# Performance work log

Hardware: AMD Instinct MI355X
Metric: run time of the kernel (lower is better)

Reference implementation:

```python
import jax, jax.numpy as jnp
import numpy as np

B, N, C, H, KHOP = 8, 1024, 512, 16, 2
HD = C // H
VALID = 768          # valid (non-padded) nodes per batch row
E = B * VALID * 32   # ~deg 32 per valid node
BN_EPS = 1e-5
LN_EPS = 1e-5


def setup_inputs() -> dict:
    key = jax.random.key(0)
    ks = jax.random.split(key, 12)
    x = jax.random.normal(ks[0], (B, N, C), jnp.float32)
    shift = jax.random.normal(ks[1], (B, C), jnp.float32) * 0.1
    scale = jax.random.normal(ks[2], (B, C), jnp.float32) * 0.1
    # fixed-size valid prefix per row -> static shapes under jit
    mask = jnp.broadcast_to(jnp.arange(N) < VALID, (B, N))
    # edges live inside a single graph (same batch row), only among valid nodes,
    # expressed directly in flattened [B*N] index space (== compacted indexing up to relabeling)
    eb = jax.random.randint(ks[3], (E,), 0, B)
    es = jax.random.randint(ks[4], (E,), 0, VALID)
    ed = jax.random.randint(ks[5], (E,), 0, VALID)
    edge_index = jnp.stack([eb * N + es, eb * N + ed]).astype(jnp.int32)
    w = lambda k, s: jax.random.normal(k, s, jnp.float32) * 0.02
    gin_eps = jnp.zeros((KHOP,), jnp.float32)
    gin_w1 = w(ks[6], (KHOP, C, 2 * C)); gin_b1 = jnp.zeros((KHOP, 2 * C), jnp.float32)
    gin_bn_g = jnp.ones((KHOP, 2 * C), jnp.float32); gin_bn_b = jnp.zeros((KHOP, 2 * C), jnp.float32)
    gin_w2 = w(ks[7], (KHOP, 2 * C, C)); gin_b2 = jnp.zeros((KHOP, C), jnp.float32)
    ln_g = jnp.ones((C,), jnp.float32); ln_b = jnp.zeros((C,), jnp.float32)
    qkv_w = w(ks[8], (C, 3 * C)); qkv_b = jnp.zeros((3 * C,), jnp.float32)
    proj_w = w(ks[9], (C, C)); proj_b = jnp.zeros((C,), jnp.float32)
    return dict(x=x, shift=shift, scale=scale, mask=mask, edge_index=edge_index,
                gin_eps=gin_eps, gin_w1=gin_w1, gin_b1=gin_b1, gin_bn_g=gin_bn_g,
                gin_bn_b=gin_bn_b, gin_w2=gin_w2, gin_b2=gin_b2, ln_g=ln_g, ln_b=ln_b,
                qkv_w=qkv_w, qkv_b=qkv_b, proj_w=proj_w, proj_b=proj_b)


def _gin_layer(h, mask_f, cnt, src, dst, eps, w1, b1, g, bt, w2, b2):
    # GINConv: mlp((1+eps)*x_i + sum_{j->i} x_j); MLP = Linear->BatchNorm(batch stats over valid nodes)->ReLU->Linear
    agg = jax.ops.segment_sum(h[src], dst, num_segments=B * N)  # scatter-add messages
    z = (1.0 + eps) * h + agg
    pre = z @ w1 + b1                              # [B*N, 2C]
    mw = mask_f[:, None]
    mean = (pre * mw).sum(0) / cnt                 # masked BN statistics (valid nodes only)
    var = (((pre - mean) ** 2) * mw).sum(0) / cnt  # biased var, as torch BatchNorm
    hn = jax.nn.relu(g * (pre - mean) * jax.lax.rsqrt(var + BN_EPS) + bt)
    return (hn @ w2 + b2) * mw                     # zero out padded nodes (x_struct stays 0 there)


def reference(x, shift, scale, mask, edge_index, gin_eps, gin_w1, gin_b1, gin_bn_g,
              gin_bn_b, gin_w2, gin_b2, ln_g, ln_b, qkv_w, qkv_b, proj_w, proj_b):
    xf = x.reshape(B * N, C)
    mask_f = mask.reshape(-1).astype(x.dtype)
    cnt = mask_f.sum()
    src, dst = edge_index[0], edge_index[1]
    # structure extractor: k-hop GIN with residual after the first hop
    h = _gin_layer(xf * mask_f[:, None], mask_f, cnt, src, dst, gin_eps[0],
                   gin_w1[0], gin_b1[0], gin_bn_g[0], gin_bn_b[0], gin_w2[0], gin_b2[0])
    for i in range(1, KHOP):
        h = _gin_layer(h, mask_f, cnt, src, dst, gin_eps[i],
                       gin_w1[i], gin_b1[i], gin_bn_g[i], gin_bn_b[i], gin_w2[i], gin_b2[i]) + h
    xs = x + h.reshape(B, N, C)  # x + x_struct (x_struct zero on padded nodes)
    # LayerNorm + modulate
    mu = xs.mean(-1, keepdims=True)
    va = xs.var(-1, keepdims=True)
    xn = (xs - mu) * jax.lax.rsqrt(va + LN_EPS) * ln_g + ln_b
    xm = xn * (1.0 + scale[:, None, :]) + shift[:, None, :]
    # SDPA attention with key padding mask
    qkv = (xm @ qkv_w + qkv_b).reshape(B, N, 3, H, HD).transpose(2, 0, 3, 1, 4)
    q, k, v = qkv[0], qkv[1], qkv[2]                       # [B,H,N,HD]
    scores = jnp.einsum('bhqd,bhkd->bhqk', q, k) * (HD ** -0.5)
    scores = scores + jnp.where(mask[:, None, None, :], 0.0, -1e9)
    attn = jax.nn.softmax(scores, axis=-1)
    out = jnp.einsum('bhqk,bhkd->bhqd', attn, v).transpose(0, 2, 1, 3).reshape(B, N, C)
    return out @ proj_w + proj_b
```

## Files before the change

### kernel.cpp

```cpp
#include <hip/hip_runtime.h>
#include <hip/hip_bf16.h>

constexpr int Bc    = 8;
constexpr int Nn    = 1024;
constexpr int Cc    = 512;
constexpr int Hh    = 16;
constexpr int HD    = 32;
constexpr int VALID = 768;
constexpr float CNT_INV = 1.0f / 6144.0f;
constexpr float BN_EPS = 1e-5f;
constexpr float LN_EPS = 1e-5f;
constexpr int ROWS = Bc * Nn;
constexpr int VROWS = Bc * VALID;
constexpr float QSCL = 0.25500526764086547f;

typedef short s16x8 __attribute__((ext_vector_type(8)));
typedef float f32x4 __attribute__((ext_vector_type(4)));

static __device__ __forceinline__ unsigned short f2bf(float f) {
    __hip_bfloat16 h = __float2bfloat16(f);
    return *reinterpret_cast<unsigned short*>(&h);
}
static __device__ __forceinline__ float bf2f(unsigned short u) {
    union { unsigned int u; float f; } c; c.u = (unsigned int)u << 16;
    return c.f;
}
static __device__ __forceinline__ float exp2_fast(float x) {
    float r; asm("v_exp_f32 %0, %1" : "=v"(r) : "v"(x)); return r;
}

static __device__ __forceinline__ int vswz(int d) {
    return ((((d >> 3) ^ (d >> 1)) & 3) << 1) | (d & 1);
}

__global__ __launch_bounds__(256) void k_wt_all(const float* __restrict__ gw1,
                                                const float* __restrict__ gw2,
                                                const float* __restrict__ qkvw,
                                                const float* __restrict__ projw,
                                                const float* __restrict__ x,
                                                unsigned short* __restrict__ w1t,
                                                unsigned short* __restrict__ w2t,
                                                unsigned short* __restrict__ qkvt,
                                                unsigned short* __restrict__ projt,
                                                unsigned short* __restrict__ xb,
                                                float* __restrict__ stats,
                                                int* __restrict__ ideg) {
    const int bi = blockIdx.x;
    if (bi >= 3072) {
        int e = (bi - 3072) * 2048 + threadIdx.x * 8;
        float4 a = *(const float4*)&x[e];
        float4 b = *(const float4*)&x[e + 4];
        s16x8 o;
        o[0] = (short)f2bf(a.x); o[1] = (short)f2bf(a.y);
        o[2] = (short)f2bf(a.z); o[3] = (short)f2bf(a.w);
        o[4] = (short)f2bf(b.x); o[5] = (short)f2bf(b.y);
        o[6] = (short)f2bf(b.z); o[7] = (short)f2bf(b.w);
        *(s16x8*)&xb[e] = o;
        return;
    }
    if (bi == 0) {
        for (int i = threadIdx.x; i < 4096; i += 256) stats[i] = 0.f;
    } else if (bi == 1) {
        for (int i = threadIdx.x; i < 8192; i += 256) ideg[i] = 0;
    }

    const float* W; unsigned short* Wt; int K, N, bx, by;
    if (bi < 1024) {
        int z = bi >> 9, r = bi & 511;
        W = gw1 + (size_t)z * 524288; Wt = w1t + (size_t)z * 524288;
        K = 512; N = 1024; bx = r & 31; by = r >> 5;
    } else if (bi < 2048) {
        int z = (bi - 1024) >> 9, r = (bi - 1024) & 511;
        W = gw2 + (size_t)z * 524288; Wt = w2t + (size_t)z * 524288;
        K = 1024; N = 512; bx = r & 15; by = r >> 4;
    } else if (bi < 2816) {
        int r = bi - 2048;
        W = qkvw; Wt = qkvt; K = 512; N = 1536; bx = r % 48; by = r / 48;
    } else {
        int r = bi - 2816;
        W = projw; Wt = projt; K = 512; N = 512; bx = r & 15; by = r >> 4;
    }

    __shared__ float t[32][33];
    const int k0 = by * 32, n0 = bx * 32;
    int kk = threadIdx.x >> 3, nn = (threadIdx.x & 7) * 4;
    float4 v = *(const float4*)&W[(size_t)(k0 + kk) * N + n0 + nn];
    t[kk][nn] = v.x; t[kk][nn + 1] = v.y; t[kk][nn + 2] = v.z; t[kk][nn + 3] = v.w;
    __syncthreads();
    int nn2 = threadIdx.x >> 3, kk2 = (threadIdx.x & 7) * 4;
    ushort4 o;
    o.x = f2bf(t[kk2][nn2]);     o.y = f2bf(t[kk2 + 1][nn2]);
    o.z = f2bf(t[kk2 + 2][nn2]); o.w = f2bf(t[kk2 + 3][nn2]);
    *(ushort4*)&Wt[(size_t)(n0 + nn2) * K + k0 + kk2] = o;
}

__global__ __launch_bounds__(256) void k_count(const int* __restrict__ ei,
                                               int* __restrict__ deg, int E) {
    int e = blockIdx.x * 256 + threadIdx.x;
    if (e < E) atomicAdd(&deg[ei[E + e]], 1);
}

__global__ __launch_bounds__(1024) void k_scan(const int* __restrict__ deg,
                                               int* __restrict__ start,
                                               int* __restrict__ cursor) {
    __shared__ int csum[1024];
    const int t = threadIdx.x;
    const int base = t * 8;
    int local[8];
    int s = 0;
#pragma unroll
    for (int i = 0; i < 8; ++i) { local[i] = deg[base + i]; s += local[i]; }
    csum[t] = s;
    __syncthreads();
    for (int off = 1; off < 1024; off <<= 1) {
        int v = (t >= off) ? csum[t - off] : 0;
        __syncthreads();
        if (t >= off) csum[t] += v;
        __syncthreads();
    }
    int excl = (t == 0) ? 0 : csum[t - 1];
#pragma unroll
    for (int i = 0; i < 8; ++i) {
        start[base + i]  = excl;
        cursor[base + i] = excl;
        excl += local[i];
    }
    if (t == 1023) start[8192] = excl;
}

__global__ __launch_bounds__(256) void k_fill(const int* __restrict__ ei,
                                              int* __restrict__ cursor,
                                              int* __restrict__ list, int E) {
    int e = blockIdx.x * 256 + threadIdx.x;
    if (e < E) {
        int pos = atomicAdd(&cursor[ei[E + e]], 1);
        list[pos] = ei[e];
    }
}

__global__ __launch_bounds__(64) void k_gather_z(const unsigned short* __restrict__ h,
                                                 const int* __restrict__ start,
                                                 const int* __restrict__ list,
                                                 const float* __restrict__ epsArr,
                                                 int layer,
                                                 unsigned short* __restrict__ z) {
    const int vr = blockIdx.x;
    const int batch = vr / 768;
    const int row = batch * 1024 + (vr - batch * 768);
    const int c = threadIdx.x * 8;
    const int s0 = start[row], s1 = start[row + 1];
    const float e1 = 1.0f + epsArr[layer];
    const unsigned short* hp = h + c;
    s16x8 bv = *(const s16x8*)&h[(size_t)row * 512 + c];
    float a[8];
#pragma unroll
    for (int i = 0; i < 8; ++i) a[i] = bf2f((unsigned short)bv[i]) * e1;
    int j = s0;
    for (; j + 4 <= s1; j += 4) {
        int sA = list[j], sB = list[j + 1], sC = list[j + 2], sD = list[j + 3];
        s16x8 vA = *(const s16x8*)&hp[(size_t)sA * 512];
        s16x8 vB = *(const s16x8*)&hp[(size_t)sB * 512];
        s16x8 vC = *(const s16x8*)&hp[(size_t)sC * 512];
        s16x8 vD = *(const s16x8*)&hp[(size_t)sD * 512];
#pragma unroll
        for (int i = 0; i < 8; ++i) {
            a[i] += bf2f((unsigned short)vA[i]);
            a[i] += bf2f((unsigned short)vB[i]);
            a[i] += bf2f((unsigned short)vC[i]);
            a[i] += bf2f((unsigned short)vD[i]);
        }
    }
    for (; j < s1; ++j) {
        s16x8 vA = *(const s16x8*)&hp[(size_t)list[j] * 512];
#pragma unroll
        for (int i = 0; i < 8; ++i) a[i] += bf2f((unsigned short)vA[i]);
    }
    s16x8 o;
#pragma unroll
    for (int i = 0; i < 8; ++i) o[i] = (short)f2bf(a[i]);
    *(s16x8*)&z[(size_t)row * 512 + c] = o;
}

template <bool RESIDUAL, bool STATS, bool SKIPM, bool OUTBF, bool QSCALE,
          bool HBF, bool SKIPKV, int BNSZ>
__global__ __launch_bounds__(256) void k_gemm_bf(const unsigned short* __restrict__ A,
                                                 const unsigned short* __restrict__ Bt,
                                                 const float* __restrict__ bias,
                                                 const float* __restrict__ res,
                                                 void* __restrict__ Cd,
                                                 float* __restrict__ stats,
                                                 unsigned short* __restrict__ hb,
                                                 int K, int Nc) {
    __shared__ unsigned short Al[128 * 64];
    __shared__ unsigned short Bl[BNSZ * 64];
    constexpr int NF = BNSZ / 32;
    constexpr int NB = (BNSZ == 128) ? 4 : 2;
    const int tid  = threadIdx.x;
    const int by   = blockIdx.y;
    const int bm   = SKIPM ? ((by / 6) * 1024 + (by % 6) * 128) : (by * 128);
    const int bn   = blockIdx.x * BNSZ;
    if (SKIPKV && (by & 7) >= 6 && bn >= 512) return;
    const int wid  = tid >> 6, lane = tid & 63;
    const int wr   = wid >> 1, wc = wid & 1;
    const int lo16 = lane & 15, g = lane >> 4;

    const int sr = tid >> 1, sh = tid & 1;
    const size_t a_off = (size_t)(bm + sr) * K + sh * 32;
    const int srb = (BNSZ == 128) ? (tid >> 1) : (tid >> 2);
    const int shb = (BNSZ == 128) ? (tid & 1)  : (tid & 3);
    const size_t b_off = (size_t)(bn + srb) * K + shb * (BNSZ == 128 ? 32 : 16);

    f32x4 acc[4][NF];
#pragma unroll
    for (int m = 0; m < 4; ++m)
#pragma unroll
        for (int n = 0; n < NF; ++n) acc[m][n] = (f32x4){0.f, 0.f, 0.f, 0.f};

    const int NT = K >> 6;
    s16x8 ar[4], br[NB];
    {
        const s16x8* ap = (const s16x8*)(A + a_off);
        const s16x8* bp = (const s16x8*)(Bt + b_off);
#pragma unroll
        for (int i = 0; i < 4; ++i)  ar[i] = ap[i];
#pragma unroll
        for (int i = 0; i < NB; ++i) br[i] = bp[i];
    }

    for (int kt = 0; kt < NT; ++kt) {
        __syncthreads();
#pragma unroll
        for (int i = 0; i < 4; ++i) {
            int sl = (sh * 4 + i) ^ (sr & 7);
            *(s16x8*)&Al[sr * 64 + sl * 8] = ar[i];
        }
#pragma unroll
        for (int i = 0; i < NB; ++i) {
            int s = (BNSZ == 128) ? (shb * 4 + i) : (shb * 2 + i);
            int sl = s ^ (srb & 7);
            *(s16x8*)&Bl[srb * 64 + sl * 8] = br[i];
        }
        __syncthreads();
        if (kt + 1 < NT) {
            const s16x8* ap = (const s16x8*)(A + a_off + (size_t)(kt + 1) * 64);
            const s16x8* bp = (const s16x8*)(Bt + b_off + (size_t)(kt + 1) * 64);
#pragma unroll
            for (int i = 0; i < 4; ++i)  ar[i] = ap[i];
#pragma unroll
            for (int i = 0; i < NB; ++i) br[i] = bp[i];
        }
#pragma unroll
        for (int ks = 0; ks < 2; ++ks) {
            s16x8 af[4], bfr[NF];
#pragma unroll
            for (int m = 0; m < 4; ++m) {
                int r = wr * 64 + m * 16 + lo16;
                int sl = (ks * 4 + g) ^ (r & 7);
                af[m] = *(const s16x8*)&Al[r * 64 + sl * 8];
            }
#pragma unroll
            for (int n = 0; n < NF; ++n) {
                int r = wc * (BNSZ / 2) + n * 16 + lo16;
                int sl = (ks * 4 + g) ^ (r & 7);
                bfr[n] = *(const s16x8*)&Bl[r * 64 + sl * 8];
            }
            __builtin_amdgcn_s_setprio(1);
#pragma unroll
            for (int m = 0; m < 4; ++m)
#pragma unroll
                for (int n = 0; n < NF; ++n)
                    acc[m][n] = __builtin_amdgcn_mfma_f32_16x16x32_bf16(
                        af[m], bfr[n], acc[m][n], 0, 0, 0);
            __builtin_amdgcn_s_setprio(0);
        }
    }

#pragma unroll
    for (int n = 0; n < NF; ++n) {
        int col = bn + wc * (BNSZ / 2) + n * 16 + lo16;
        float bb = bias[col];
        bool qs = QSCALE && (col < 512);
        float s = 0.f, s2 = 0.f;
#pragma unroll
        for (int m = 0; m < 4; ++m) {
#pragma unroll
            for (int ri = 0; ri < 4; ++ri) {
                int row = bm + wr * 64 + m * 16 + g * 4 + ri;
                float v = acc[m][n][ri] + bb;
                if (STATS) { s += v; s2 += v * v; }
                if (RESIDUAL) v += res[(size_t)row * Nc + col];
                if (QSCALE && qs) v *= QSCL;
                if (OUTBF) ((unsigned short*)Cd)[(size_t)row * Nc + col] = f2bf(v);
                else       ((float*)Cd)[(size_t)row * Nc + col] = v;
                if (HBF)   hb[(size_t)row * Nc + col] = f2bf(v);
            }
        }
        if (STATS) {
            s  += __shfl_xor(s, 16);  s  += __shfl_xor(s, 32);
            s2 += __shfl_xor(s2, 16); s2 += __shfl_xor(s2, 32);
            if (g == 0) {
                atomicAdd(&stats[col], s);
                atomicAdd(&stats[1024 + col], s2);
            }
        }
    }
}

__global__ __launch_bounds__(128) void k_bn_apply(const unsigned short* __restrict__ pre,
                                                  const float* __restrict__ stats,
                                                  const float* __restrict__ g,
                                                  const float* __restrict__ bt,
                                                  unsigned short* __restrict__ hn) {
    const int vr = blockIdx.x;
    const int batch = vr / 768;
    const int row = batch * 1024 + (vr - batch * 768);
    const int c0 = threadIdx.x * 8;
    const size_t off = (size_t)row * 1024 + c0;
    s16x8 v = *(const s16x8*)&pre[off];
    s16x8 o;
#pragma unroll
    for (int i = 0; i < 8; ++i) {
        float sm = stats[c0 + i], sq = stats[1024 + c0 + i];
        float m = sm * CNT_INV;
        float r = rsqrtf(sq * CNT_INV - m * m + BN_EPS);
        float hv = g[c0 + i] * (bf2f((unsigned short)v[i]) - m) * r + bt[c0 + i];
        o[i] = (short)f2bf(fmaxf(hv, 0.f));
    }
    *(s16x8*)&hn[off] = o;
}

__global__ __launch_bounds__(256) void k_ln_mod(const float* __restrict__ x,
                                                const float* __restrict__ h,
                                                const float* __restrict__ lg,
                                                const float* __restrict__ lb,
                                                const float* __restrict__ sc,
                                                const float* __restrict__ sh,
                                                unsigned short* __restrict__ xm) {
    int row  = blockIdx.x * 4 + (threadIdx.x >> 6);
    int lane = threadIdx.x & 63;
    const size_t base = (size_t)row * 512 + lane * 8;
    const bool val = (row & 1023) < VALID;

    float v[8];
    float4 a0 = *(const float4*)&x[base],     a1 = *(const float4*)&x[base + 4];
    float4 b0 = *(const float4*)&h[base],     b1 = *(const float4*)&h[base + 4];
    if (!val) { b0.x=b0.y=b0.z=b0.w=0.f; b1.x=b1.y=b1.z=b1.w=0.f; }
    v[0] = a0.x + b0.x; v[1] = a0.y + b0.y; v[2] = a0.z + b0.z; v[3] = a0.w + b0.w;
    v[4] = a1.x + b1.x; v[5] = a1.y + b1.y; v[6] = a1.z + b1.z; v[7] = a1.w + b1.w;

    float s = 0.f, s2 = 0.f;
#pragma unroll
    for (int j = 0; j < 8; ++j) { s += v[j]; s2 += v[j] * v[j]; }
#pragma unroll
    for (int off = 32; off; off >>= 1) {
        s  += __shfl_xor(s, off);
        s2 += __shfl_xor(s2, off);
    }
    float mu  = s * (1.0f / 512.0f);
    float var = s2 * (1.0f / 512.0f) - mu * mu;
    float rs  = rsqrtf(var + LN_EPS);

    int c0 = lane * 8;
    int bidx = row >> 10;
    const float* scp = sc + (size_t)bidx * 512 + c0;
    const float* shp = sh + (size_t)bidx * 512 + c0;
    s16x8 o;
#pragma unroll
    for (int j = 0; j < 8; ++j) {
        float xn = (v[j] - mu) * rs * lg[c0 + j] + lb[c0 + j];
        o[j] = (short)f2bf(xn * (1.0f + scp[j]) + shp[j]);
    }
    *(s16x8*)&xm[base] = o;
}

__global__ __launch_bounds__(256) void k_attn_mfma(const unsigned short* __restrict__ qkv,
                                                   unsigned short* __restrict__ att) {
    __shared__ __align__(16) unsigned short Kl[128 * 32];
    __shared__ __align__(16) unsigned short Vt[32 * 128];
    __shared__ __align__(16) unsigned short Pl[4][16 * 128];

    const int w    = threadIdx.x >> 6;
    const int lane = threadIdx.x & 63;
    const int bh   = blockIdx.x;
    const int b    = bh >> 4, h = bh & 15;
    const int qt   = blockIdx.y;
    const int lo16 = lane & 15;
    const int g    = lane >> 4;

    const int qrowA = qt * 128 + w * 16 + lo16;
    s16x8 qfa = *(const s16x8*)&qkv[(size_t)(b * 1024 + qrowA) * 1536 + h * 32 + g * 8];
    s16x8 qfb = *(const s16x8*)&qkv[(size_t)(b * 1024 + qrowA + 64) * 1536 + h * 32 + g * 8];

    f32x4 o0a = {0.f,0.f,0.f,0.f}, o1a = {0.f,0.f,0.f,0.f};
    f32x4 o0b = {0.f,0.f,0.f,0.f}, o1b = {0.f,0.f,0.f,0.f};
    float la = 0.f, lb = 0.f;

    const size_t kvbase = (size_t)(b * 1024) * 1536 + h * 32;

    const int kr_r = threadIdx.x >> 2;
    const int kr_g = threadIdx.x & 3;
    const int vk0  = (threadIdx.x >> 2) * 2;
    const int vgg  = threadIdx.x & 3;

    s16x8 kA, kB, vA, vB;
    {
        const unsigned short* kp = &qkv[kvbase + (size_t)kr_r * 1536 + 512 + kr_g * 8];
        kA = *(const s16x8*)kp;
        kB = *(const s16x8*)(kp + (size_t)64 * 1536);
        const unsigned short* vp = &qkv[kvbase + (size_t)vk0 * 1536 + 1024 + vgg * 8];
        vA = *(const s16x8*)vp;
        vB = *(const s16x8*)(vp + 1536);
    }

    for (int kc = 0; kc < VALID; kc += 128) {
        __syncthreads();

        {
            int slot = kr_g ^ ((kr_r >> 1) & 3);
            *(s16x8*)&Kl[kr_r * 32 + slot * 8] = kA;
            int r2 = 64 + kr_r;
            slot = kr_g ^ ((r2 >> 1) & 3);
            *(s16x8*)&Kl[r2 * 32 + slot * 8] = kB;
        }
#pragma unroll
        for (int j = 0; j < 8; ++j) {
            int d = vgg * 8 + j;
            int slot = (vk0 >> 3) ^ vswz(d);
            int elem = d * 128 + slot * 8 + (vk0 & 7);
            unsigned int pack = (unsigned int)(unsigned short)vA[j] |
                                ((unsigned int)(unsigned short)vB[j] << 16);
            *(unsigned int*)&Vt[elem] = pack;
        }
        __syncthreads();

        if (kc + 128 < VALID) {
            const unsigned short* kp = &qkv[kvbase + (size_t)(kc + 128 + kr_r) * 1536 + 512 + kr_g * 8];
            kA = *(const s16x8*)kp;
            kB = *(const s16x8*)(kp + (size_t)64 * 1536);
            const unsigned short* vp = &qkv[kvbase + (size_t)(kc + 128 + vk0) * 1536 + 1024 + vgg * 8];
            vA = *(const s16x8*)vp;
            vB = *(const s16x8*)(vp + 1536);
        }

        f32x4 sc[8];
        __builtin_amdgcn_s_setprio(1);
#pragma unroll
        for (int t = 0; t < 8; ++t) {
            int r = t * 16 + lo16;
            int slot = g ^ ((r >> 1) & 3);
            s16x8 kf = *(const s16x8*)&Kl[r * 32 + slot * 8];
            f32x4 z = {0.f, 0.f, 0.f, 0.f};
            sc[t] = __builtin_amdgcn_mfma_f32_16x16x32_bf16(kf, qfa, z, 0, 0, 0);
        }
        __builtin_amdgcn_s_setprio(0);

        {
            float lsum = 0.f;
#pragma unroll
            for (int t = 0; t < 8; ++t) {
                float p0 = exp2_fast(sc[t][0]);
                float p1 = exp2_fast(sc[t][1]);
                float p2 = exp2_fast(sc[t][2]);
                float p3 = exp2_fast(sc[t][3]);
                lsum += (p0 + p1) + (p2 + p3);
                int kstart = t * 16 + g * 4;
                int slot = (kstart >> 3) ^ (lo16 & 7);
                int elem = lo16 * 128 + slot * 8 + (kstart & 7);
                unsigned int lo = (unsigned int)f2bf(p0) | ((unsigned int)f2bf(p1) << 16);
                unsigned int hi = (unsigned int)f2bf(p2) | ((unsigned int)f2bf(p3) << 16);
                uint2 pk; pk.x = lo; pk.y = hi;
                *(uint2*)&Pl[w][elem] = pk;
            }
            la += lsum;
        }

        f32x4 sd[8];
        __builtin_amdgcn_s_setprio(1);
#pragma unroll
        for (int t = 0; t < 8; ++t) {
            int r = t * 16 + lo16;
            int slot = g ^ ((r >> 1) & 3);
            s16x8 kf = *(const s16x8*)&Kl[r * 32 + slot * 8];
            f32x4 z = {0.f, 0.f, 0.f, 0.f};
            sd[t] = __builtin_amdgcn_mfma_f32_16x16x32_bf16(kf, qfb, z, 0, 0, 0);
        }
        __builtin_amdgcn_s_setprio(0);

        asm volatile("s_waitcnt lgkmcnt(0)" ::: "memory");
        __builtin_amdgcn_sched_barrier(0);

        __builtin_amdgcn_s_setprio(1);
#pragma unroll
        for (int sub = 0; sub < 4; ++sub) {
            int slotp = (sub * 4 + g) ^ (lo16 & 7);
            s16x8 pa = *(const s16x8*)&Pl[w][lo16 * 128 + slotp * 8];
            int d0 = lo16;
            s16x8 vb0 = *(const s16x8*)&Vt[d0 * 128 + (((sub * 4 + g) ^ vswz(d0)) * 8)];
            int d1 = 16 + lo16;
            s16x8 vb1 = *(const s16x8*)&Vt[d1 * 128 + (((sub * 4 + g) ^ vswz(d1)) * 8)];
            o0a = __builtin_amdgcn_mfma_f32_16x16x32_bf16(pa, vb0, o0a, 0, 0, 0);
            o1a = __builtin_amdgcn_mfma_f32_16x16x32_bf16(pa, vb1, o1a, 0, 0, 0);
        }
        __builtin_amdgcn_s_setprio(0);

        {
            float lsum = 0.f;
#pragma unroll
            for (int t = 0; t < 8; ++t) {
                float p0 = exp2_fast(sd[t][0]);
                float p1 = exp2_fast(sd[t][1]);
                float p2 = exp2_fast(sd[t][2]);
                float p3 = exp2_fast(sd[t][3]);
                lsum += (p0 + p1) + (p2 + p3);
                int kstart = t * 16 + g * 4;
                int slot = (kstart >> 3) ^ (lo16 & 7);
                int elem = lo16 * 128 + slot * 8 + (kstart & 7);
                unsigned int lo = (unsigned int)f2bf(p0) | ((unsigned int)f2bf(p1) << 16);
                unsigned int hi = (unsigned int)f2bf(p2) | ((unsigned int)f2bf(p3) << 16);
                uint2 pk; pk.x = lo; pk.y = hi;
                *(uint2*)&Pl[w][elem] = pk;
            }
            lb += lsum;
        }

        asm volatile("s_waitcnt lgkmcnt(0)" ::: "memory");
        __builtin_amdgcn_sched_barrier(0);

        __builtin_amdgcn_s_setprio(1);
#pragma unroll
        for (int sub = 0; sub < 4; ++sub) {
            int slotp = (sub * 4 + g) ^ (lo16 & 7);
            s16x8 pa = *(const s16x8*)&Pl[w][lo16 * 128 + slotp * 8];
            int d0 = lo16;
            s16x8 vb0 = *(const s16x8*)&Vt[d0 * 128 + (((sub * 4 + g) ^ vswz(d0)) * 8)];
            int d1 = 16 + lo16;
            s16x8 vb1 = *(const s16x8*)&Vt[d1 * 128 + (((sub * 4 + g) ^ vswz(d1)) * 8)];
            o0b = __builtin_amdgcn_mfma_f32_16x16x32_bf16(pa, vb0, o0b, 0, 0, 0);
            o1b = __builtin_amdgcn_mfma_f32_16x16x32_bf16(pa, vb1, o1b, 0, 0, 0);
        }
        __builtin_amdgcn_s_setprio(0);
    }

#pragma unroll
    for (int qi = 0; qi < 2; ++qi) {
        float l = qi ? lb : la;
        l += __shfl_xor(l, 16);
        l += __shfl_xor(l, 32);
#pragma unroll
        for (int r = 0; r < 4; ++r) {
            float lr = __shfl(l, g * 4 + r);
            float inv = 1.f / lr;
            int qq = qt * 128 + qi * 64 + w * 16 + g * 4 + r;
            unsigned short* op = att + ((size_t)(b * 1024 + qq) * 512 + h * 32);
            float v0 = (qi ? o0b[r] : o0a[r]) * inv;
            float v1 = (qi ? o1b[r] : o1a[r]) * inv;
            op[lo16]      = f2bf(v0);
            op[16 + lo16] = f2bf(v1);
        }
    }
}

extern "C" void kernel_launch(void* const* d_in, const int* in_sizes, int n_in,
                              void* d_out, int out_size, void* d_ws, size_t ws_size,
                              hipStream_t stream) {
    const float* x     = (const float*)d_in[0];
    const float* shift = (const float*)d_in[1];
    const float* scale = (const float*)d_in[2];
    const int*   ei    = (const int*)d_in[4];
    const float* geps  = (const float*)d_in[5];
    const float* gw1   = (const float*)d_in[6];
    const float* gb1   = (const float*)d_in[7];
    const float* gbg   = (const float*)d_in[8];
    const float* gbb   = (const float*)d_in[9];
    const float* gw2   = (const float*)d_in[10];
    const float* gb2   = (const float*)d_in[11];
    const float* lng   = (const float*)d_in[12];
    const float* lnb   = (const float*)d_in[13];
    const float* qkvw  = (const float*)d_in[14];
    const float* qkvb  = (const float*)d_in[15];
    const float* projw = (const float*)d_in[16];
    const float* projb = (const float*)d_in[17];
    const int E = in_sizes[4] / 2;

    float* ws    = (float*)d_ws;
    float* bufA  = ws;
    float* bufB  = ws + 4194304;
    float* preq  = ws + 8388608;
    float* stats = ws + 20971520;
    int*   ideg    = (int*)(ws + 20975616);
    int*   istart  = ideg + 8192;
    int*   icursor = istart + 8193;
    int*   ilist   = icursor + 8192;
    unsigned short* hnb = (unsigned short*)(ws + 16777216);
    unsigned short* wts = (unsigned short*)(ws + 21200896);
    unsigned short* w1t   = wts;
    unsigned short* w2t   = wts + 1048576;
    unsigned short* qkvt  = wts + 2097152;
    unsigned short* projt = wts + 2883584;
    unsigned short* xb  = (unsigned short*)preq;
    unsigned short* hb  = (unsigned short*)(preq + 2097152);
    unsigned short* pre = (unsigned short*)preq;

    k_wt_all<<<5120, 256, 0, stream>>>(gw1, gw2, qkvw, projw, x,
                                       w1t, w2t, qkvt, projt, xb, stats, ideg);

    k_count<<<(E + 255) / 256, 256, 0, stream>>>(ei, ideg, E);
    k_scan<<<1, 1024, 0, stream>>>(ideg, istart, icursor);
    k_fill<<<(E + 255) / 256, 256, 0, stream>>>(ei, icursor, ilist, E);

    for (int layer = 0; layer < 2; ++layer) {
        const unsigned short* hin = layer ? hb : xb;
        unsigned short* zb = (unsigned short*)(layer ? bufA : bufB);
        float* st = stats + layer * 2048;
        k_gather_z<<<VROWS, 64, 0, stream>>>(hin, istart, ilist, geps, layer, zb);
        k_gemm_bf<false, true, true, true, false, false, false, 64>
            <<<dim3(16, 48), 256, 0, stream>>>(
            zb, w1t + (size_t)layer * 524288, gb1 + layer * 1024, nullptr,
            pre, st, nullptr, 512, 1024);
        k_bn_apply<<<VROWS, 128, 0, stream>>>(pre, st, gbg + layer * 1024,
                                              gbb + layer * 1024, hnb);
        if (layer == 0) {
            k_gemm_bf<false, false, true, false, false, true, false, 64>
                <<<dim3(8, 48), 256, 0, stream>>>(
                hnb, w2t, gb2, nullptr, bufB, nullptr, hb, 1024, 512);
        } else {
            k_gemm_bf<true, false, true, false, false, false, false, 64>
                <<<dim3(8, 48), 256, 0, stream>>>(
                hnb, w2t + 524288, gb2 + 512, bufB, bufA, nullptr, nullptr, 1024, 512);
        }
    }

    unsigned short* xmb = (unsigned short*)bufB;
    k_ln_mod<<<2048, 256, 0, stream>>>(x, bufA, lng, lnb, scale, shift, xmb);
    unsigned short* qkvb16 = (unsigned short*)preq;
    k_gemm_bf<false, false, false, true, true, false, true, 128>
        <<<dim3(12, 64), 256, 0, stream>>>(
        xmb, qkvt, qkvb, nullptr, qkvb16, nullptr, nullptr, 512, 1536);
    unsigned short* attb = (unsigned short*)bufA;
    k_attn_mfma<<<dim3(128, 8), 256, 0, stream>>>(qkvb16, attb);
    k_gemm_bf<false, false, false, false, false, false, false, 64>
        <<<dim3(8, 64), 256, 0, stream>>>(
        attb, projt, projb, nullptr, (float*)d_out, nullptr, nullptr, 512, 512);
}
```

Measured before the change: 230.1 us.

## Store GIN hidden states in bf16, convert only valid x rows, interleave gather order

The second GIN linear layer now writes its hidden output only as bf16 instead of both fp32 and bf16. The second layer's residual is read from bf16, and LayerNorm reads h from bf16. The x-to-bf16 conversion now covers only valid rows, so fewer blocks are launched. The gather and BN kernels interleave batches across block indices so neighbouring blocks touch different graphs. This cuts fp32 traffic and redundant writes, at the cost of extra bf16 rounding in the residual path.

```diff
diff --git a/kernel.cpp b/kernel.cpp
--- a/kernel.cpp
+++ b/kernel.cpp
@@ -47,7 +47,10 @@
                                                 int* __restrict__ ideg) {
     const int bi = blockIdx.x;
     if (bi >= 3072) {
-        int e = (bi - 3072) * 2048 + threadIdx.x * 8;
+        int vr4 = (bi - 3072) * 4;
+        int batch = vr4 / 768;
+        int row = batch * 1024 + (vr4 - batch * 768);
+        size_t e = (size_t)row * 512 + threadIdx.x * 8;
         float4 a = *(const float4*)&x[e];
         float4 b = *(const float4*)&x[e + 4];
         s16x8 o;
@@ -145,8 +148,8 @@
                                                  int layer,
                                                  unsigned short* __restrict__ z) {
     const int vr = blockIdx.x;
-    const int batch = vr / 768;
-    const int row = batch * 1024 + (vr - batch * 768);
+    const int batch = vr & 7;
+    const int row = batch * 1024 + (vr >> 3);
     const int c = threadIdx.x * 8;
     const int s0 = start[row], s1 = start[row + 1];
     const float e1 = 1.0f + epsArr[layer];
@@ -182,14 +185,13 @@
 }
 
 template <bool RESIDUAL, bool STATS, bool SKIPM, bool OUTBF, bool QSCALE,
-          bool HBF, bool SKIPKV, int BNSZ>
+          bool RESBF, bool SKIPKV, int BNSZ>
 __global__ __launch_bounds__(256) void k_gemm_bf(const unsigned short* __restrict__ A,
                                                  const unsigned short* __restrict__ Bt,
                                                  const float* __restrict__ bias,
-                                                 const float* __restrict__ res,
+                                                 const void* __restrict__ res,
                                                  void* __restrict__ Cd,
                                                  float* __restrict__ stats,
-                                                 unsigned short* __restrict__ hb,
                                                  int K, int Nc) {
     __shared__ unsigned short Al[128 * 64];
     __shared__ unsigned short Bl[BNSZ * 64];
@@ -288,11 +290,15 @@
                 int row = bm + wr * 64 + m * 16 + g * 4 + ri;
                 float v = acc[m][n][ri] + bb;
                 if (STATS) { s += v; s2 += v * v; }
-                if (RESIDUAL) v += res[(size_t)row * Nc + col];
+                if (RESIDUAL) {
+                    if (RESBF)
+                        v += bf2f(((const unsigned short*)res)[(size_t)row * Nc + col]);
+                    else
+                        v += ((const float*)res)[(size_t)row * Nc + col];
+                }
                 if (QSCALE && qs) v *= QSCL;
                 if (OUTBF) ((unsigned short*)Cd)[(size_t)row * Nc + col] = f2bf(v);
                 else       ((float*)Cd)[(size_t)row * Nc + col] = v;
-                if (HBF)   hb[(size_t)row * Nc + col] = f2bf(v);
             }
         }
         if (STATS) {
@@ -312,8 +318,8 @@
                                                   const float* __restrict__ bt,
                                                   unsigned short* __restrict__ hn) {
     const int vr = blockIdx.x;
-    const int batch = vr / 768;
-    const int row = batch * 1024 + (vr - batch * 768);
+    const int batch = vr & 7;
+    const int row = batch * 1024 + (vr >> 3);
     const int c0 = threadIdx.x * 8;
     const size_t off = (size_t)row * 1024 + c0;
     s16x8 v = *(const s16x8*)&pre[off];
@@ -330,7 +336,7 @@
 }
 
 __global__ __launch_bounds__(256) void k_ln_mod(const float* __restrict__ x,
-                                                const float* __restrict__ h,
+                                                const unsigned short* __restrict__ h,
                                                 const float* __restrict__ lg,
                                                 const float* __restrict__ lb,
                                                 const float* __restrict__ sc,
@@ -342,11 +348,14 @@
     const bool val = (row & 1023) < VALID;
 
     float v[8];
-    float4 a0 = *(const float4*)&x[base],     a1 = *(const float4*)&x[base + 4];
-    float4 b0 = *(const float4*)&h[base],     b1 = *(const float4*)&h[base + 4];
-    if (!val) { b0.x=b0.y=b0.z=b0.w=0.f; b1.x=b1.y=b1.z=b1.w=0.f; }
-    v[0] = a0.x + b0.x; v[1] = a0.y + b0.y; v[2] = a0.z + b0.z; v[3] = a0.w + b0.w;
-    v[4] = a1.x + b1.x; v[5] = a1.y + b1.y; v[6] = a1.z + b1.z; v[7] = a1.w + b1.w;
+    float4 a0 = *(const float4*)&x[base], a1 = *(const float4*)&x[base + 4];
+    s16x8 hv8 = *(const s16x8*)&h[base];
+    float xa[8] = {a0.x, a0.y, a0.z, a0.w, a1.x, a1.y, a1.z, a1.w};
+#pragma unroll
+    for (int j = 0; j < 8; ++j) {
+        float hj = val ? bf2f((unsigned short)hv8[j]) : 0.f;
+        v[j] = xa[j] + hj;
+    }
 
     float s = 0.f, s2 = 0.f;
 #pragma unroll
@@ -583,8 +592,6 @@
     const int E = in_sizes[4] / 2;
 
     float* ws    = (float*)d_ws;
-    float* bufA  = ws;
-    float* bufB  = ws + 4194304;
     float* preq  = ws + 8388608;
     float* stats = ws + 20971520;
     int*   ideg    = (int*)(ws + 20975616);
@@ -597,11 +604,17 @@
     unsigned short* w2t   = wts + 1048576;
     unsigned short* qkvt  = wts + 2097152;
     unsigned short* projt = wts + 2883584;
-    unsigned short* xb  = (unsigned short*)preq;
-    unsigned short* hb  = (unsigned short*)(preq + 2097152);
-    unsigned short* pre = (unsigned short*)preq;
-
-    k_wt_all<<<5120, 256, 0, stream>>>(gw1, gw2, qkvw, projw, x,
+    unsigned short* xb   = (unsigned short*)preq;
+    unsigned short* pre  = (unsigned short*)preq;
+    unsigned short* zb0  = (unsigned short*)(ws + 4194304);
+    unsigned short* hb   = (unsigned short*)(ws + 6291456);
+    unsigned short* zb1  = (unsigned short*)ws;
+    unsigned short* h2b  = (unsigned short*)(ws + 2097152);
+    unsigned short* xmb  = (unsigned short*)(ws + 4194304);
+    unsigned short* qkvb16 = (unsigned short*)preq;
+    unsigned short* attb = (unsigned short*)ws;
+
+    k_wt_all<<<4608, 256, 0, stream>>>(gw1, gw2, qkvw, projw, x,
                                        w1t, w2t, qkvt, projt, xb, stats, ideg);
 
     k_count<<<(E + 255) / 256, 256, 0, stream>>>(ei, ideg, E);
@@ -610,35 +623,32 @@
 
     for (int layer = 0; layer < 2; ++layer) {
         const unsigned short* hin = layer ? hb : xb;
-        unsigned short* zb = (unsigned short*)(layer ? bufA : bufB);
+        unsigned short* zb = layer ? zb1 : zb0;
         float* st = stats + layer * 2048;
         k_gather_z<<<VROWS, 64, 0, stream>>>(hin, istart, ilist, geps, layer, zb);
         k_gemm_bf<false, true, true, true, false, false, false, 64>
             <<<dim3(16, 48), 256, 0, stream>>>(
             zb, w1t + (size_t)layer * 524288, gb1 + layer * 1024, nullptr,
-            pre, st, nullptr, 512, 1024);
+            pre, st, 512, 1024);
         k_bn_apply<<<VROWS, 128, 0, stream>>>(pre, st, gbg + layer * 1024,
                                               gbb + layer * 1024, hnb);
         if (layer == 0) {
-            k_gemm_bf<false, false, true, false, false, true, false, 64>
+            k_gemm_bf<false, false, true, true, false, false, false, 64>
                 <<<dim3(8, 48), 256, 0, stream>>>(
-                hnb, w2t, gb2, nullptr, bufB, nullptr, hb, 1024, 512);
+                hnb, w2t, gb2, nullptr, hb, nullptr, 1024, 512);
         } else {
-            k_gemm_bf<true, false, true, false, false, false, false, 64>
+            k_gemm_bf<true, false, true, true, false, true, false, 64>
                 <<<dim3(8, 48), 256, 0, stream>>>(
-                hnb, w2t + 524288, gb2 + 512, bufB, bufA, nullptr, nullptr, 1024, 512);
-        }
-    }
-
-    unsigned short* xmb = (unsigned short*)bufB;
-    k_ln_mod<<<2048, 256, 0, stream>>>(x, bufA, lng, lnb, scale, shift, xmb);
-    unsigned short* qkvb16 = (unsigned short*)preq;
+                hnb, w2t + 524288, gb2 + 512, hb, h2b, nullptr, 1024, 512);
+        }
+    }
+
+    k_ln_mod<<<2048, 256, 0, stream>>>(x, h2b, lng, lnb, scale, shift, xmb);
     k_gemm_bf<false, false, false, true, true, false, true, 128>
         <<<dim3(12, 64), 256, 0, stream>>>(
-        xmb, qkvt, qkvb, nullptr, qkvb16, nullptr, nullptr, 512, 1536);
-    unsigned short* attb = (unsigned short*)bufA;
+        xmb, qkvt, qkvb, nullptr, qkvb16, nullptr, 512, 1536);
     k_attn_mfma<<<dim3(128, 8), 256, 0, stream>>>(qkvb16, attb);
     k_gemm_bf<false, false, false, false, false, false, false, 64>
         <<<dim3(8, 64), 256, 0, stream>>>(
-        attb, projt, projb, nullptr, (float*)d_out, nullptr, nullptr, 512, 512);
-}
+        attb, projt, projb, nullptr, (float*)d_out, nullptr, 512, 512);
+}
```

Result: faster. 212.9 us (-7.5%).
